# Kernel optimization log

Measured on AMD Instinct MI355X. Metric: run time of the kernel, lower is better.

Reference implementation:

```python
import jax, jax.numpy as jnp
import numpy as np

D = 128      # internal_dimensions
L = 4        # num_edge_convs
N = 100000   # nodes
E = 800000   # edges
G = 64       # graphs
IN = 4       # in_channels


def _ln(x, g, b):
    m = jnp.mean(x, -1, keepdims=True)
    v = jnp.mean((x - m) ** 2, -1, keepdims=True)
    return (x - m) * jax.lax.rsqrt(v + 1e-5) * g + b


def _gelu(x):
    return jax.nn.gelu(x, approximate=False)  # torch nn.GELU default (erf)


def _seg_mean(x, seg, n):
    s = jax.ops.segment_sum(x, seg, num_segments=n)
    c = jax.ops.segment_sum(jnp.ones((x.shape[0], 1), x.dtype), seg, num_segments=n)
    return s / jnp.maximum(c, 1.0)


def _seg_max(x, seg, n):
    m = jax.ops.segment_max(x, seg, num_segments=n)
    return jnp.where(jnp.isfinite(m), m, 0.0)  # empty segments -> 0 (PyG convention)


def _forward(x, edge_index, batch, num_graphs,
             in_W1, in_b1, in_g1, in_bn1, in_W2, in_b2, in_g2, in_bn2,
             pre_g, pre_b, cW1, cb1, cg1, cbb1, cW2, cb2, cg2, cbb2, pW, pb,
             ag_g, ag_b,
             kW1, kb1, kg1, kbb1, kW2, kb2, kg2, kbb2,
             kW3, kb3, kg3, kbb3, kW4, kb4):
    n = x.shape[0]
    # input_net: Linear -> LN -> GELU -> Linear -> LN   (dropout=0, eval)
    h = _gelu(_ln(x @ in_W1 + in_b1, in_g1, in_bn1))
    h = _ln(h @ in_W2 + in_b2, in_g2, in_bn2)

    x_in_max = _seg_max(h, batch, num_graphs)
    x_in_mean = _seg_mean(h, batch, num_graphs)

    src, dst = edge_index[0], edge_index[1]  # PyG: message from src (x_j) to dst (x_i)
    xcur = h
    for l in range(L):
        identity = xcur
        hn = _ln(xcur, pre_g[l], pre_b[l])
        xi = hn[dst]            # [E, D]
        xj = hn[src]            # [E, D]
        m = jnp.concatenate([xi, xj - xi], axis=-1)       # [E, 2D]
        m = _gelu(_ln(m @ cW1[l] + cb1[l], cg1[l], cbb1[l]))
        m = _gelu(_ln(m @ cW2[l] + cb2[l], cg2[l], cbb2[l]))
        a_max = _seg_max(m, dst, n)
        a_mean = _seg_mean(m, dst, n)
        aggr = jnp.concatenate([a_max, a_mean], axis=-1)  # [N, 2D]
        xcur = identity + aggr @ pW[l] + pb[l]

    xcur = _ln(xcur, ag_g, ag_b)
    x_g_max = _seg_max(xcur, batch, num_graphs)
    x_g_mean = _seg_mean(xcur, batch, num_graphs)

    xp = jnp.concatenate([x_in_max, x_in_mean, x_g_max, x_g_mean], axis=-1)  # [G, 4D]
    z = _gelu(_ln(xp @ kW1 + kb1, kg1, kbb1))
    z = _gelu(_ln(z @ kW2 + kb2, kg2, kbb2))
    z = _gelu(_ln(z @ kW3 + kb3, kg3, kbb3))
    return z @ kW4 + kb4  # [G, 1]


def setup_inputs() -> dict:
    key = jax.random.key(0)
    ks = iter(jax.random.split(key, 64))
    def W(shape, fan):
        return jax.random.normal(next(ks), shape, jnp.float32) * np.float32((2.0 / fan) ** 0.5)
    inp = {}
    inp["x"] = jax.random.normal(next(ks), (N, IN), jnp.float32)
    inp["edge_index"] = jax.random.randint(next(ks), (2, E), 0, N)
    inp["batch"] = jnp.sort(jax.random.randint(next(ks), (N,), 0, G))
    inp["num_graphs"] = G
    inp["in_W1"] = W((IN, D), IN); inp["in_b1"] = jnp.zeros((D,), jnp.float32)
    inp["in_g1"] = jnp.ones((D,), jnp.float32); inp["in_bn1"] = jnp.zeros((D,), jnp.float32)
    inp["in_W2"] = W((D, D), D); inp["in_b2"] = jnp.zeros((D,), jnp.float32)
    inp["in_g2"] = jnp.ones((D,), jnp.float32); inp["in_bn2"] = jnp.zeros((D,), jnp.float32)
    inp["pre_g"] = jnp.ones((L, D), jnp.float32); inp["pre_b"] = jnp.zeros((L, D), jnp.float32)
    inp["cW1"] = W((L, 2 * D, D), 2 * D); inp["cb1"] = jnp.zeros((L, D), jnp.float32)
    inp["cg1"] = jnp.ones((L, D), jnp.float32); inp["cbb1"] = jnp.zeros((L, D), jnp.float32)
    inp["cW2"] = W((L, D, D), D); inp["cb2"] = jnp.zeros((L, D), jnp.float32)
    inp["cg2"] = jnp.ones((L, D), jnp.float32); inp["cbb2"] = jnp.zeros((L, D), jnp.float32)
    inp["pW"] = W((L, 2 * D, D), 2 * D); inp["pb"] = jnp.zeros((L, D), jnp.float32)
    inp["ag_g"] = jnp.ones((D,), jnp.float32); inp["ag_b"] = jnp.zeros((D,), jnp.float32)
    inp["kW1"] = W((4 * D, D), 4 * D); inp["kb1"] = jnp.zeros((D,), jnp.float32)
    inp["kg1"] = jnp.ones((D,), jnp.float32); inp["kbb1"] = jnp.zeros((D,), jnp.float32)
    inp["kW2"] = W((D, D), D); inp["kb2"] = jnp.zeros((D,), jnp.float32)
    inp["kg2"] = jnp.ones((D,), jnp.float32); inp["kbb2"] = jnp.zeros((D,), jnp.float32)
    inp["kW3"] = W((D, D // 4), D); inp["kb3"] = jnp.zeros((D // 4,), jnp.float32)
    inp["kg3"] = jnp.ones((D // 4,), jnp.float32); inp["kbb3"] = jnp.zeros((D // 4,), jnp.float32)
    inp["kW4"] = W((D // 4, 1), D // 4); inp["kb4"] = jnp.zeros((1,), jnp.float32)
    return inp


def reference(x, edge_index, batch, num_graphs,
              in_W1, in_b1, in_g1, in_bn1, in_W2, in_b2, in_g2, in_bn2,
              pre_g, pre_b, cW1, cb1, cg1, cbb1, cW2, cb2, cg2, cbb2, pW, pb,
              ag_g, ag_b,
              kW1, kb1, kg1, kbb1, kW2, kb2, kg2, kbb2,
              kW3, kb3, kg3, kbb3, kW4, kb4):
    return _forward(x, edge_index, batch, num_graphs,
                    in_W1, in_b1, in_g1, in_bn1, in_W2, in_b2, in_g2, in_bn2,
                    pre_g, pre_b, cW1, cb1, cg1, cbb1, cW2, cb2, cg2, cbb2, pW, pb,
                    ag_g, ag_b,
                    kW1, kb1, kg1, kbb1, kW2, kb2, kg2, kbb2,
                    kW3, kb3, kg3, kbb3, kW4, kb4)
```

## Files before the change

### kernel.cpp

```cpp
#include <hip/hip_runtime.h>
#include <hip/hip_bf16.h>
#include <math.h>

__device__ __forceinline__ float geluf(float x) {
    return 0.5f * x * (1.0f + erff(x * 0.70710678118654752f));
}
#define MAPNEGINF 0x007FFFFFu
__device__ __forceinline__ float funmap(unsigned m) {
    return __uint_as_float((m & 0x80000000u) ? (m ^ 0x80000000u) : ~m);
}
__device__ __forceinline__ unsigned fmap(float f) {
    unsigned u = __float_as_uint(f);
    return ((int)u < 0) ? ~u : (u | 0x80000000u);
}
__device__ __forceinline__ float wred64(float v) {
#pragma unroll
    for (int m = 1; m < 64; m <<= 1) v += __shfl_xor(v, m);
    return v;
}
__device__ __forceinline__ unsigned short bf16r(float f) {
    unsigned u = __float_as_uint(f);
    u += 0x7fffu + ((u >> 16) & 1u);
    return (unsigned short)(u >> 16);
}

__device__ __forceinline__ void stage_wq(float* Ws, const float* __restrict__ src, int t) {
#pragma unroll
    for (int it = 0; it < 4; ++it) {
        const int idx = it * 1024 + (t << 2);
        *(float4*)(Ws + idx) = *(const float4*)(src + idx);
    }
}

__device__ __forceinline__ void stage_w2(float* Ws, const float* __restrict__ base,
                                         const float* __restrict__ sub, int t) {
#pragma unroll
    for (int it = 0; it < 4; ++it) {
        const int idx = it * 1024 + (t << 2);
        float4 v = *(const float4*)(base + idx);
        if (sub) {
            const float4 s = *(const float4*)(sub + idx);
            v = make_float4(v.x - s.x, v.y - s.y, v.z - s.z, v.w - s.w);
        }
        *(float4*)(Ws + idx) = v;
    }
}

__device__ __forceinline__ void kloop_q(const float* As, const float* Ws, float (&acc)[4][8],
                                        const int r0, const int ogc, const int kb) {
#pragma unroll
    for (int kk = 0; kk < 32; kk += 4) {
        const float4 a0 = *(const float4*)(As + (r0 + 0) * 132 + kb + kk);
        const float4 a1 = *(const float4*)(As + (r0 + 1) * 132 + kb + kk);
        const float4 a2 = *(const float4*)(As + (r0 + 2) * 132 + kb + kk);
        const float4 a3 = *(const float4*)(As + (r0 + 3) * 132 + kb + kk);
#define MAD8(R, AV)                                                                     \
    {                                                                                   \
        acc[R][0] += (AV)*wA.x; acc[R][1] += (AV)*wA.y; acc[R][2] += (AV)*wA.z;         \
        acc[R][3] += (AV)*wA.w; acc[R][4] += (AV)*wB.x; acc[R][5] += (AV)*wB.y;         \
        acc[R][6] += (AV)*wB.z; acc[R][7] += (AV)*wB.w;                                 \
    }
#define KSTEP(J, C)                                                                     \
    {                                                                                   \
        const float4 wA = *(const float4*)(Ws + (kk + (J)) * 128 + ogc);                \
        const float4 wB = *(const float4*)(Ws + (kk + (J)) * 128 + 64 + ogc);           \
        MAD8(0, a0.C) MAD8(1, a1.C) MAD8(2, a2.C) MAD8(3, a3.C)                         \
    }
        KSTEP(0, x) KSTEP(1, y) KSTEP(2, z) KSTEP(3, w)
#undef KSTEP
#undef MAD8
    }
}

__device__ __forceinline__ void kloop2(const float* As, const float* Ws, float (&acc)[2][8],
                                       const int r0, const int ogc, const int kb) {
#pragma unroll
    for (int kk = 0; kk < 32; kk += 4) {
        const float4 a0 = *(const float4*)(As + (r0 + 0) * 132 + kb + kk);
        const float4 a1 = *(const float4*)(As + (r0 + 1) * 132 + kb + kk);
#define MAD8(R, AV)                                                                     \
    {                                                                                   \
        acc[R][0] += (AV)*wA.x; acc[R][1] += (AV)*wA.y; acc[R][2] += (AV)*wA.z;         \
        acc[R][3] += (AV)*wA.w; acc[R][4] += (AV)*wB.x; acc[R][5] += (AV)*wB.y;         \
        acc[R][6] += (AV)*wB.z; acc[R][7] += (AV)*wB.w;                                 \
    }
#define KSTEP(J, C)                                                                     \
    {                                                                                   \
        const float4 wA = *(const float4*)(Ws + (kk + (J)) * 128 + ogc);                \
        const float4 wB = *(const float4*)(Ws + (kk + (J)) * 128 + 64 + ogc);           \
        MAD8(0, a0.C) MAD8(1, a1.C)                                                     \
    }
        KSTEP(0, x) KSTEP(1, y) KSTEP(2, z) KSTEP(3, w)
#undef KSTEP
#undef MAD8
    }
}

__global__ void k_zero(unsigned* __restrict__ p, int n) {
    const int i = blockIdx.x * 256 + threadIdx.x;
    if (i < n) p[i] = 0u;
}

__global__ void k_copyu(const unsigned* __restrict__ a, const unsigned* __restrict__ b,
                        unsigned* __restrict__ ac, unsigned* __restrict__ bc, int n) {
    const int i = blockIdx.x * 256 + threadIdx.x;
    if (i < n) {
        ac[i] = a[i];
        bc[i] = b[i];
    }
}

__global__ void k_count(const int* __restrict__ ei, unsigned* __restrict__ deg, int E) {
    const int e = blockIdx.x * 256 + threadIdx.x;
// ... 95 lines not shown
                                                const float* __restrict__ bias,
                                                const float* __restrict__ g,
                                                const float* __restrict__ b,
                                                float* __restrict__ C, int n) {
    __shared__ float As[32 * 132];
    __shared__ float Ws[4096];
    const int t = threadIdx.x;
    const int n0 = blockIdx.x * 32;
    {
        const int r = t >> 3, c0 = (t & 7) << 4;
        const int row = n0 + r;
        const bool ok = row < n;
#pragma unroll
        for (int j = 0; j < 4; ++j) {
            const int col = c0 + (j << 2);
            float4 v = make_float4(0.f, 0.f, 0.f, 0.f);
            if (ok) v = *(const float4*)(A + (size_t)row * 128 + col);
            *(float4*)(As + r * 132 + col) = v;
        }
    }
    float acc[2][8];
#pragma unroll
    for (int r = 0; r < 2; ++r)
#pragma unroll
        for (int o = 0; o < 8; ++o) acc[r][o] = 0.f;
    const int og = t & 15, eg = t >> 4;
    const int ogc = og << 2, r0 = eg << 1;
#pragma unroll
    for (int q4 = 0; q4 < 4; ++q4) {
        stage_wq(Ws, W + q4 * 4096, t);
        __syncthreads();
        kloop2(As, Ws, acc, r0, ogc, q4 * 32);
        __syncthreads();
    }
    const float4 bA = *(const float4*)(bias + ogc);
    const float4 bB = *(const float4*)(bias + 64 + ogc);
    const float4 gA = *(const float4*)(g + ogc);
    const float4 gB = *(const float4*)(g + 64 + ogc);
    const float4 lA = *(const float4*)(b + ogc);
    const float4 lB = *(const float4*)(b + 64 + ogc);
#pragma unroll
    for (int r = 0; r < 2; ++r) {
        float v[8];
        v[0] = acc[r][0] + bA.x; v[1] = acc[r][1] + bA.y;
        v[2] = acc[r][2] + bA.z; v[3] = acc[r][3] + bA.w;
        v[4] = acc[r][4] + bB.x; v[5] = acc[r][5] + bB.y;
        v[6] = acc[r][6] + bB.z; v[7] = acc[r][7] + bB.w;
        float s = 0.f, q = 0.f;
#pragma unroll
        for (int o = 0; o < 8; ++o) { s += v[o]; q += v[o] * v[o]; }
#pragma unroll
        for (int m = 1; m < 16; m <<= 1) { s += __shfl_xor(s, m); q += __shfl_xor(q, m); }
        const float mean = s * 0.0078125f;
        const float var = q * 0.0078125f - mean * mean;
        const float rs = rsqrtf(var + 1e-5f);
        const int row = n0 + r0 + r;
        if (row < n) {
            *(float4*)(C + (size_t)row * 128 + ogc) = make_float4(
                (v[0] - mean) * rs * gA.x + lA.x, (v[1] - mean) * rs * gA.y + lA.y,
                (v[2] - mean) * rs * gA.z + lA.z, (v[3] - mean) * rs * gA.w + lA.w);
            *(float4*)(C + (size_t)row * 128 + 64 + ogc) = make_float4(
                (v[4] - mean) * rs * gB.x + lB.x, (v[5] - mean) * rs * gB.y + lB.y,
                (v[6] - mean) * rs * gB.z + lB.z, (v[7] - mean) * rs * gB.w + lB.w);
        }
    }
}

__global__ void k_ln(const float* __restrict__ in, const float* __restrict__ g,
                     const float* __restrict__ b, float* __restrict__ out, int n) {
    const int t = threadIdx.x, lane = t & 63, wave = t >> 6;
    const int d0 = lane << 1;
    const float ga = g[d0], gb = g[d0 + 1], ba = b[d0], bb = b[d0 + 1];
    const int stride = gridDim.x * 4;
    for (int node = blockIdx.x * 4 + wave; node < n; node += stride) {
        const float2 v = *(const float2*)(in + (size_t)node * 128 + d0);
        const float s = wred64(v.x + v.y), q = wred64(v.x * v.x + v.y * v.y);
        const float mean = s * 0.0078125f, var = q * 0.0078125f - mean * mean;
        const float rs = rsqrtf(var + 1e-5f);
        *(float2*)(out + (size_t)node * 128 + d0) =
            make_float2((v.x - mean) * rs * ga + ba, (v.y - mean) * rs * gb + bb);
    }
}

__global__ __launch_bounds__(256, 4) void k_gemmh(const float* __restrict__ A,
                                                  const float* __restrict__ g,
                                                  const float* __restrict__ b,
                                                  const float* __restrict__ wbase,
                                                  const float* __restrict__ wsub,
                                                  const float* __restrict__ bias,
                                                  unsigned short* __restrict__ C, int n) {
    __shared__ float As[32 * 132];
    __shared__ float Ws[4096];
    __shared__ float sg[128], sb[128];
    const int t = threadIdx.x;
    const int n0 = blockIdx.x * 32;
    if (t < 128) { sg[t] = g[t]; sb[t] = b[t]; }
    __syncthreads();
    {
        const int r = t >> 3, c0 = (t & 7) << 4;
        const int row = n0 + r;
        const bool ok = row < n;
        float4 v4[4];
        float s = 0.f, q = 0.f;
        if (ok) {
#pragma unroll
            for (int j = 0; j < 4; ++j) {
                v4[j] = *(const float4*)(A + (size_t)row * 128 + c0 + (j << 2));
                s += v4[j].x + v4[j].y + v4[j].z + v4[j].w;
                q += v4[j].x * v4[j].x + v4[j].y * v4[j].y + v4[j].z * v4[j].z +
                     v4[j].w * v4[j].w;
            }
        } else {
#pragma unroll
            for (int j = 0; j < 4; ++j) v4[j] = make_float4(0.f, 0.f, 0.f, 0.f);
        }
        s += __shfl_xor(s, 1); s += __shfl_xor(s, 2); s += __shfl_xor(s, 4);
        q += __shfl_xor(q, 1); q += __shfl_xor(q, 2); q += __shfl_xor(q, 4);
        const float mean = s * 0.0078125f;
        const float var = q * 0.0078125f - mean * mean;
        const float rs = rsqrtf(var + 1e-5f);
#pragma unroll
        for (int j = 0; j < 4; ++j) {
            const int c = c0 + (j << 2);
            As[r * 132 + c + 0] = (v4[j].x - mean) * rs * sg[c + 0] + sb[c + 0];
            As[r * 132 + c + 1] = (v4[j].y - mean) * rs * sg[c + 1] + sb[c + 1];
            As[r * 132 + c + 2] = (v4[j].z - mean) * rs * sg[c + 2] + sb[c + 2];
            As[r * 132 + c + 3] = (v4[j].w - mean) * rs * sg[c + 3] + sb[c + 3];
        }
    }
    float acc[2][8];
#pragma unroll
    for (int r = 0; r < 2; ++r)
#pragma unroll
        for (int o = 0; o < 8; ++o) acc[r][o] = 0.f;
    const int og = t & 15, eg = t >> 4;
    const int ogc = og << 2, r0 = eg << 1;
#pragma unroll
    for (int q4 = 0; q4 < 4; ++q4) {
        stage_w2(Ws, wbase + q4 * 4096, wsub ? (wsub + q4 * 4096) : (const float*)nullptr, t);
        __syncthreads();
        kloop2(As, Ws, acc, r0, ogc, q4 * 32);
        __syncthreads();
    }
    float4 bA = make_float4(0.f, 0.f, 0.f, 0.f), bB = bA;
    if (bias) {
        bA = *(const float4*)(bias + ogc);
        bB = *(const float4*)(bias + 64 + ogc);
    }
#pragma unroll
    for (int r = 0; r < 2; ++r) {
        const int row = n0 + r0 + r;
        if (row < n) {
            ushort4 u0, u1;
            u0.x = bf16r(acc[r][0] + bA.x); u0.y = bf16r(acc[r][1] + bA.y);
            u0.z = bf16r(acc[r][2] + bA.z); u0.w = bf16r(acc[r][3] + bA.w);
            u1.x = bf16r(acc[r][4] + bB.x); u1.y = bf16r(acc[r][5] + bB.y);
            u1.z = bf16r(acc[r][6] + bB.z); u1.w = bf16r(acc[r][7] + bB.w);
            *(ushort4*)(C + (size_t)row * 128 + ogc) = u0;
            *(ushort4*)(C + (size_t)row * 128 + 64 + ogc) = u1;
        }
    }
}

__global__ __launch_bounds__(256, 2) void k_edge(
    const unsigned short* __restrict__ P, const unsigned short* __restrict__ Q,
    const int* __restrict__ esrc, const int* __restrict__ edst, const float* __restrict__ W2,
    const float* __restrict__ g1, const float* __restrict__ b1, const float* __restrict__ cb2,
    const float* __restrict__ g2, const float* __restrict__ b2,
    const unsigned* __restrict__ rowend, const unsigned* __restrict__ degc,
    float* __restrict__ amax, float* __restrict__ asum, float* __restrict__ recmax,
    float* __restrict__ recsum, int* __restrict__ recid, int E) {
    __shared__ float Us[64 * 132];
    __shared__ float Ws[4096];
    __shared__ int sdst[64], ssrc[64], sdg[64];
    __shared__ float scb2[128], sg2[128], sb2[128];
    const int t = threadIdx.x;
    const int base = blockIdx.x * 512;
    if (t >= 128) {
        const int d = t - 128;
        scb2[d] = cb2[d];
        sg2[d] = g2[d];
        sb2[d] = b2[d];
    }
    const int lane = t & 63, wave = t >> 6;
    const int d0 = lane << 1;
    const float g1a = g1[d0], g1b = g1[d0 + 1], b1a = b1[d0], b1b = b1[d0 + 1];
    const int og = t & 15, eg = t >> 4;
    const int ogc = og << 2, r0 = eg << 2;
    int cur = -1, istart = 0;
    float vmax = -INFINITY, vsum = 0.f;
    int id0 = -1, id1 = -1;

    for (int s8 = 0; s8 < 8; ++s8) {
        const int sb = base + s8 * 64;
        __syncthreads();
        if (t < 64) {
            const int idx = sb + t;
            const int ci = idx < E ? idx : (E - 1);
            ssrc[t] = esrc[ci];
            const int d = edst[ci];
            sdg[t] = d;
            sdst[t] = (idx < E) ? d : -1;
        }
        __syncthreads();
#pragma unroll 4
        for (int p = 0; p < 16; ++p) {
            const int i = (p << 2) + wave;
            const unsigned pu = *(const unsigned*)(P + ((size_t)sdg[i] << 7) + d0);
            const unsigned qu = *(const unsigned*)(Q + ((size_t)ssrc[i] << 7) + d0);
            const float x0 = __uint_as_float(pu << 16) + __uint_as_float(qu << 16);
            const float x1 =
                __uint_as_float(pu & 0xffff0000u) + __uint_as_float(qu & 0xffff0000u);
            const float s = wred64(x0 + x1);
            const float q = wred64(x0 * x0 + x1 * x1);
            const float mean = s * 0.0078125f;
            const float var = q * 0.0078125f - mean * mean;
            const float rs = rsqrtf(var + 1e-5f);
            const float y0 = geluf((x0 - mean) * rs * g1a + b1a);
            const float y1 = geluf((x1 - mean) * rs * g1b + b1b);
            *(float2*)(Us + i * 132 + d0) = make_float2(y0, y1);
        }
        float acc[4][8];
#pragma unroll
        for (int r = 0; r < 4; ++r)
#pragma unroll
            for (int o = 0; o < 8; ++o) acc[r][o] = 0.f;
#pragma unroll
        for (int q4 = 0; q4 < 4; ++q4) {
            stage_wq(Ws, W2 + q4 * 4096, t);
            __syncthreads();
            kloop_q(Us, Ws, acc, r0, ogc, q4 * 32);
            __syncthreads();
        }
#pragma unroll
        for (int r = 0; r < 4; ++r) {
            float v[8];
            float s = 0.f, q = 0.f;
#pragma unroll
            for (int o = 0; o < 8; ++o) {
                const int col = (o < 4) ? (ogc + o) : (64 + ogc + o - 4);
                v[o] = acc[r][o] + scb2[col];
                s += v[o];
                q += v[o] * v[o];
            }
#pragma unroll
            for (int m = 1; m < 16; m <<= 1) { s += __shfl_xor(s, m); q += __shfl_xor(q, m); }
            const float mean = s * 0.0078125f;
            const float var = q * 0.0078125f - mean * mean;
            const float rs = rsqrtf(var + 1e-5f);
#pragma unroll
            for (int o = 0; o < 8; ++o) {
                const int col = (o < 4) ? (ogc + o) : (64 + ogc + o - 4);
                v[o] = geluf((v[o] - mean) * rs * sg2[col] + sb2[col]);
            }
            *(float4*)(Us + (r0 + r) * 132 + ogc) = make_float4(v[0], v[1], v[2], v[3]);
            *(float4*)(Us + (r0 + r) * 132 + 64 + ogc) = make_float4(v[4], v[5], v[6], v[7]);
        }
        __syncthreads();
        if (t < 128) {
            for (int i = 0; i < 64; ++i) {
                const int dn = sdst[i];
                const int gi = s8 * 64 + i;
                if (dn != cur) {
                    if (cur >= 0) {
                        const unsigned re = rowend[cur];
                        const unsigned rs0 = re - degc[cur];
                        const unsigned ps = (unsigned)(base + istart);
                        const unsigned pe = (unsigned)(base + gi);
                        if (ps == rs0 && pe == re) {
                            amax[(size_t)cur * 128 + t] = vmax;
                            asum[(size_t)cur * 128 + t] = vsum;
                        } else {
                            const int slot = (istart == 0) ? 0 : 1;
                            const size_t ro = (size_t)(2 * blockIdx.x + slot) * 128 + t;
                            recmax[ro] = vmax;
                            recsum[ro] = vsum;
                            if (slot == 0) id0 = cur; else id1 = cur;
                        }
                    }
                    cur = dn;
                    istart = gi;
                    vmax = -INFINITY;
                    vsum = 0.f;
                }
                if (dn >= 0) {
                    const float v = Us[i * 132 + t];
                    vmax = fmaxf(vmax, v);
                    vsum += v;
                }
            }
        }
    }
    if (t < 128 && cur >= 0) {
        const int iend = min(512, E - base);
        const unsigned re = rowend[cur];
        const unsigned rs0 = re - degc[cur];
        const unsigned ps = (unsigned)(base + istart);
        const unsigned pe = (unsigned)(base + iend);
        if (ps == rs0 && pe == re) {
            amax[(size_t)cur * 128 + t] = vmax;
            asum[(size_t)cur * 128 + t] = vsum;
        } else {
            const int slot = (istart == 0) ? 0 : 1;
            const size_t ro = (size_t)(2 * blockIdx.x + slot) * 128 + t;
            recmax[ro] = vmax;
            recsum[ro] = vsum;
            if (slot == 0) id0 = cur; else id1 = cur;
        }
    }
    if (t == 0) {
        recid[2 * blockIdx.x] = id0;
        recid[2 * blockIdx.x + 1] = id1;
    }
}

__global__ void k_merge(const unsigned* __restrict__ rowend, const unsigned* __restrict__ degc,
                        const float* __restrict__ recmax, const float* __restrict__ recsum,
                        const int* __restrict__ recid, float* __restrict__ amax,
                        float* __restrict__ asum, int n) {
    const int node = blockIdx.x * 2 + (threadIdx.x >> 7);
    const int t = threadIdx.x & 127;
    if (node >= n) return;
    const unsigned dg = degc[node];
    if (dg == 0u) {
        amax[(size_t)node * 128 + t] = 0.f;
        asum[(size_t)node * 128 + t] = 0.f;
        return;
    }
    const unsigned re = rowend[node], rs = re - dg;
    const int b0 = rs >> 9, b1 = (re - 1) >> 9;
    if (b0 == b1) return;
    float m = -INFINITY, s = 0.f;
    for (int b = b0; b <= b1; ++b) {
#pragma unroll
        for (int sl = 0; sl < 2; ++sl) {
            if (recid[2 * b + sl] == node) {
                const size_t ro = (size_t)(2 * b + sl) * 128 + t;
                m = fmaxf(m, recmax[ro]);
                s += recsum[ro];
            }
        }
    }
    amax[(size_t)node * 128 + t] = m;
    asum[(size_t)node * 128 + t] = s;
}

__global__ __launch_bounds__(256, 4) void k_update(const float* __restrict__ amax,
                                                   const float* __restrict__ asum,
                                                   const unsigned* __restrict__ degc,
                                                   const float* __restrict__ pW,
                                                   const float* __restrict__ pb,
                                                   float* __restrict__ xcur, int n) {
    __shared__ float As[32 * 132];
    __shared__ float Ws[4096];
    const int t = threadIdx.x;
    const int n0 = blockIdx.x * 32;
    const int og = t & 15, eg = t >> 4;
    const int ogc = og << 2, r0 = eg << 1;
    float acc[2][8];
#pragma unroll
    for (int r = 0; r < 2; ++r)
#pragma unroll
        for (int o = 0; o < 8; ++o) acc[r][o] = 0.f;
    const int r = t >> 3, c0 = (t & 7) << 4;
    const int row = n0 + r;
    const bool ok = row < n;
#pragma unroll
    for (int pass = 0; pass < 2; ++pass) {
        if (pass == 0) {
#pragma unroll
            for (int j = 0; j < 4; ++j) {
                const int col = c0 + (j << 2);
                float4 v = make_float4(0.f, 0.f, 0.f, 0.f);
                if (ok) v = *(const float4*)(amax + (size_t)row * 128 + col);
                *(float4*)(As + r * 132 + col) = v;
            }
        } else {
            float inv = 0.f;
            if (ok) {
                const unsigned dv = degc[row];
                inv = 1.f / (float)(dv < 1u ? 1u : dv);
            }
#pragma unroll
            for (int j = 0; j < 4; ++j) {
                const int col = c0 + (j << 2);
                float4 v = make_float4(0.f, 0.f, 0.f, 0.f);
                if (ok) {
                    const float4 sv = *(const float4*)(asum + (size_t)row * 128 + col);
                    v = make_float4(sv.x * inv, sv.y * inv, sv.z * inv, sv.w * inv);
                }
                *(float4*)(As + r * 132 + col) = v;
            }
        }
#pragma unroll
        for (int q4 = 0; q4 < 4; ++q4) {
            stage_wq(Ws, pW + (size_t)(pass * 128 + q4 * 32) * 128, t);
            __syncthreads();
            kloop2(As, Ws, acc, r0, ogc, q4 * 32);
            __syncthreads();
        }
    }
    const float4 bA = *(const float4*)(pb + ogc);
    const float4 bB = *(const float4*)(pb + 64 + ogc);
#pragma unroll
    for (int rr = 0; rr < 2; ++rr) {
        const int orow = n0 + r0 + rr;
        if (orow < n) {
            const float4 x0 = *(const float4*)(xcur + (size_t)orow * 128 + ogc);
            const float4 x1 = *(const float4*)(xcur + (size_t)orow * 128 + 64 + ogc);
            *(float4*)(xcur + (size_t)orow * 128 + ogc) =
                make_float4(x0.x + acc[rr][0] + bA.x, x0.y + acc[rr][1] + bA.y,
                            x0.z + acc[rr][2] + bA.z, x0.w + acc[rr][3] + bA.w);
            *(float4*)(xcur + (size_t)orow * 128 + 64 + ogc) =
                make_float4(x1.x + acc[rr][4] + bB.x, x1.y + acc[rr][5] + bB.y,
                            x1.z + acc[rr][6] + bB.z, x1.w + acc[rr][7] + bB.w);
        }
    }
}

__global__ void k_pool_init(unsigned* __restrict__ gmax1, float* __restrict__ gsum1,
                            unsigned* __restrict__ gcount1, unsigned* __restrict__ gmax2,
                            float* __restrict__ gsum2, unsigned* __restrict__ gcount2, int ng) {
    const int i = blockIdx.x * 256 + threadIdx.x;
    if (i < ng * 128) {
        gmax1[i] = MAPNEGINF;
        gsum1[i] = 0.f;
        gmax2[i] = MAPNEGINF;
        gsum2[i] = 0.f;
    }
    if (i < ng) {
        gcount1[i] = 0u;
        gcount2[i] = 0u;
    }
}

__global__ void k_pool(const float* __restrict__ in, const int* __restrict__ batch,
                       unsigned* __restrict__ gmax, float* __restrict__ gsum,
                       unsigned* __restrict__ gcount, int n) {
    const int t = threadIdx.x;
    if (t >= 128) return;
    const int per = (n + gridDim.x - 1) / gridDim.x;
    const int i0 = blockIdx.x * per;
    const int i1 = min(n, i0 + per);
    if (i0 >= i1) return;
    int cur = batch[i0];
    float vmax = -INFINITY, vsum = 0.f;
    unsigned cnt = 0;
    for (int i = i0; i < i1; ++i) {
        const int g = batch[i];
        if (g != cur) {
            atomicMax(gmax + (size_t)cur * 128 + t, fmap(vmax));
            atomicAdd(gsum + (size_t)cur * 128 + t, vsum);
            if (t == 0) atomicAdd(gcount + cur, cnt);
            cur = g;
            vmax = -INFINITY;
            vsum = 0.f;
            cnt = 0;
        }
        const float v = in[(size_t)i * 128 + t];
        vmax = fmaxf(vmax, v);
        vsum += v;
        cnt++;
    }
    atomicMax(gmax + (size_t)cur * 128 + t, fmap(vmax));
    atomicAdd(gsum + (size_t)cur * 128 + t, vsum);
    if (t == 0) atomicAdd(gcount + cur, cnt);
}

__global__ void k_xp(const unsigned* __restrict__ gmax1, const float* __restrict__ gsum1,
                     const unsigned* __restrict__ gcount1, const unsigned* __restrict__ gmax2,
                     const float* __restrict__ gsum2, const unsigned* __restrict__ gcount2,
                     float* __restrict__ xp) {
    const int g = blockIdx.x, d = threadIdx.x;
    const unsigned c1u = gcount1[g], c2u = gcount2[g];
    const float c1 = (float)(c1u < 1u ? 1u : c1u);
    const float c2 = (float)(c2u < 1u ? 1u : c2u);
    const unsigned m1 = gmax1[g * 128 + d], m2 = gmax2[g * 128 + d];
    xp[g * 512 + d] = (m1 == MAPNEGINF) ? 0.f : funmap(m1);
    xp[g * 512 + 128 + d] = gsum1[g * 128 + d] / c1;
    xp[g * 512 + 256 + d] = (m2 == MAPNEGINF) ? 0.f : funmap(m2);
    xp[g * 512 + 384 + d] = gsum2[g * 128 + d] / c2;
}

__global__ __launch_bounds__(64) void k_know(
    const float* __restrict__ xp, const float* __restrict__ kW1, const float* __restrict__ kb1,
    const float* __restrict__ kg1, const float* __restrict__ kbb1, const float* __restrict__ kW2,
    const float* __restrict__ kb2, const float* __restrict__ kg2, const float* __restrict__ kbb2,
    const float* __restrict__ kW3, const float* __restrict__ kb3, const float* __restrict__ kg3,
    const float* __restrict__ kbb3, const float* __restrict__ kW4, const float* __restrict__ kb4,
    float* __restrict__ out) {
    __shared__ float sh[512];
    __shared__ float s3[32];
    const int l = threadIdx.x, g = blockIdx.x;
    const int d0 = l << 1;
    *(float4*)(sh + l * 8) = *(const float4*)(xp + g * 512 + l * 8);
    *(float4*)(sh + l * 8 + 4) = *(const float4*)(xp + g * 512 + l * 8 + 4);
    __syncthreads();
    float a0 = kb1[d0], a1 = kb1[d0 + 1];
    for (int k = 0; k < 512; ++k) {
        const float u = sh[k];
// ... 68 lines not shown
    const int E = in_sizes[1] / 2;
    const int G = 64;
    const int L = 4;

    const float* x = (const float*)d_in[0];
    const int* ei = (const int*)d_in[1];
    const int* batch = (const int*)d_in[2];
    const float* inW1 = (const float*)d_in[4];
    const float* inb1 = (const float*)d_in[5];
    const float* ing1 = (const float*)d_in[6];
    const float* inbn1 = (const float*)d_in[7];
    const float* inW2 = (const float*)d_in[8];
    const float* inb2 = (const float*)d_in[9];
    const float* ing2 = (const float*)d_in[10];
    const float* inbn2 = (const float*)d_in[11];
    const float* pre_g = (const float*)d_in[12];
    const float* pre_b = (const float*)d_in[13];
    const float* cW1 = (const float*)d_in[14];
    const float* cb1 = (const float*)d_in[15];
    const float* cg1 = (const float*)d_in[16];
    const float* cbb1 = (const float*)d_in[17];
    const float* cW2 = (const float*)d_in[18];
    const float* cb2 = (const float*)d_in[19];
    const float* cg2 = (const float*)d_in[20];
    const float* cbb2 = (const float*)d_in[21];
    const float* pW = (const float*)d_in[22];
    const float* pb = (const float*)d_in[23];
    const float* ag_g = (const float*)d_in[24];
    const float* ag_b = (const float*)d_in[25];
    const float* kW1 = (const float*)d_in[26];
    const float* kb1 = (const float*)d_in[27];
    const float* kg1 = (const float*)d_in[28];
    const float* kbb1 = (const float*)d_in[29];
    const float* kW2 = (const float*)d_in[30];
    const float* kb2 = (const float*)d_in[31];
    const float* kg2 = (const float*)d_in[32];
    const float* kbb2 = (const float*)d_in[33];
    const float* kW3 = (const float*)d_in[34];
    const float* kb3 = (const float*)d_in[35];
    const float* kg3 = (const float*)d_in[36];
    const float* kbb3 = (const float*)d_in[37];
    const float* kW4 = (const float*)d_in[38];
    const float* kb4 = (const float*)d_in[39];
    float* out = (float*)d_out;

    const int nblkE = (E + 511) / 512;

    char* wsb = (char*)d_ws;
    size_t off = 0;
    auto ALC = [&](size_t bytes) {
        void* p = wsb + off;
        off = (off + bytes + 255) & ~(size_t)255;
        return p;
    };
    const size_t NB = (size_t)N * 128 * 4;
    float* xcur = (float*)ALC(NB);
    float* amax = (float*)ALC(NB);
    float* asum = (float*)ALC(NB);
    unsigned short* Pb = (unsigned short*)ALC((size_t)N * 128 * 2);
    unsigned short* Qb = (unsigned short*)ALC((size_t)N * 128 * 2);
    unsigned* deg = (unsigned*)ALC((size_t)N * 4);
    unsigned* cursor = (unsigned*)ALC((size_t)N * 4);
    unsigned* degc = (unsigned*)ALC((size_t)N * 4);
    unsigned* rowend = (unsigned*)ALC((size_t)N * 4);
    unsigned* bsum = (unsigned*)ALC(4096);
    int* esrc = (int*)ALC((size_t)E * 4);
    int* edst = (int*)ALC((size_t)E * 4);
    float* recmax = (float*)ALC((size_t)nblkE * 2 * 128 * 4);
    float* recsum = (float*)ALC((size_t)nblkE * 2 * 128 * 4);
    int* recid = (int*)ALC((size_t)nblkE * 2 * 4);
    unsigned* gmax1 = (unsigned*)ALC((size_t)G * 128 * 4);
    float* gsum1 = (float*)ALC((size_t)G * 128 * 4);
    unsigned* gcount1 = (unsigned*)ALC((size_t)G * 4);
    unsigned* gmax2 = (unsigned*)ALC((size_t)G * 128 * 4);
    float* gsum2 = (float*)ALC((size_t)G * 128 * 4);
    unsigned* gcount2 = (unsigned*)ALC((size_t)G * 4);
    float* xp = (float*)ALC((size_t)G * 512 * 4);

    if (off > ws_size) {
        k_zero<<<(out_size + 255) / 256, 256, 0, stream>>>((unsigned*)d_out, out_size);
        return;
    }

    k_zero<<<(N + 255) / 256, 256, 0, stream>>>(deg, N);
    k_count<<<(E + 255) / 256, 256, 0, stream>>>(ei, deg, E);
    const int nb = (N + 1023) / 1024;
    k_scan1<<<nb, 256, 0, stream>>>(deg, cursor, bsum, N);
    k_scan2<<<1, 256, 0, stream>>>(bsum, nb);
    k_scan3<<<nb, 256, 0, stream>>>(cursor, bsum, N);
    k_scatter<<<(E + 255) / 256, 256, 0, stream>>>(ei, cursor, esrc, edst, E);
    k_copyu<<<(N + 255) / 256, 256, 0, stream>>>(deg, cursor, degc, rowend, N);

    const int grid32 = (N + 31) / 32;
    k_in1<<<1024, 256, 0, stream>>>(x, inW1, inb1, ing1, inbn1, amax, N);
    k_in2<<<grid32, 256, 0, stream>>>(amax, inW2, inb2, ing2, inbn2, xcur, N);
    k_pool_init<<<(G * 128 + 255) / 256, 256, 0, stream>>>(gmax1, gsum1, gcount1, gmax2, gsum2,
                                                           gcount2, G);
    k_pool<<<512, 256, 0, stream>>>(xcur, batch, gmax1, gsum1, gcount1, N);

    for (int l = 0; l < L; ++l) {
        const float* c = cW1 + (size_t)l * 32768;
        k_gemmh<<<grid32, 256, 0, stream>>>(xcur, pre_g + l * 128, pre_b + l * 128, c,
                                            c + 16384, cb1 + l * 128, Pb, N);
        k_gemmh<<<grid32, 256, 0, stream>>>(xcur, pre_g + l * 128, pre_b + l * 128, c + 16384,
                                            (const float*)nullptr, (const float*)nullptr, Qb, N);
        k_edge<<<nblkE, 256, 0, stream>>>(Pb, Qb, esrc, edst, cW2 + (size_t)l * 16384,
                                          cg1 + l * 128, cbb1 + l * 128, cb2 + l * 128,
                                          cg2 + l * 128, cbb2 + l * 128, rowend, degc, amax, asum,
                                          recmax, recsum, recid, E);
        k_merge<<<(N + 1) / 2, 256, 0, stream>>>(rowend, degc, recmax, recsum, recid, amax, asum,
                                                 N);
        k_update<<<grid32, 256, 0, stream>>>(amax, asum, degc, pW + (size_t)l * 32768,
                                             pb + l * 128, xcur, N);
    }

    k_ln<<<1024, 256, 0, stream>>>(xcur, ag_g, ag_b, amax, N);
    k_pool<<<512, 256, 0, stream>>>(amax, batch, gmax2, gsum2, gcount2, N);
    k_xp<<<G, 128, 0, stream>>>(gmax1, gsum1, gcount1, gmax2, gsum2, gcount2, xp);
    k_know<<<G, 64, 0, stream>>>(xp, kW1, kb1, kg1, kbb1, kW2, kb2, kg2, kbb2, kW3, kb3, kg3,
                                 kbb3, kW4, kb4, out);
}
```

Before: 100.3 ms.

## Stage full weight matrices in large dynamic LDS for gemm, edge and update kernels

Adds variants of the per-layer gemm, edge-MLP and update kernels that copy the whole 128x128 weight matrix into about 97KB of dynamic shared memory once per block. This removes the per-quarter stage/sync loop, and the edge kernel reuses the staged weights across all 8 sub-tiles of its 512 edges. The gemm and update kernels also move to 64-row tiles with 4 rows per thread. The cost is fewer resident blocks per CU because of the large LDS footprint, with a fallback to the old kernels if the attribute call fails.

```diff
diff --git a/kernel.cpp b/kernel.cpp
--- a/kernel.cpp
+++ b/kernel.cpp
@@ -24,11 +24,27 @@
     return (unsigned short)(u >> 16);
 }
 
+#define DYN_LDS_BYTES 99328
+
 __device__ __forceinline__ void stage_wq(float* Ws, const float* __restrict__ src, int t) {
 #pragma unroll
     for (int it = 0; it < 4; ++it) {
         const int idx = it * 1024 + (t << 2);
         *(float4*)(Ws + idx) = *(const float4*)(src + idx);
+    }
+}
+
+__device__ __forceinline__ void stage_wfull(float* Ws, const float* __restrict__ base,
+                                            const float* __restrict__ sub, int t) {
+#pragma unroll
+    for (int it = 0; it < 16; ++it) {
+        const int idx = it * 1024 + (t << 2);
+        float4 v = *(const float4*)(base + idx);
+        if (sub) {
+            const float4 s = *(const float4*)(sub + idx);
+            v = make_float4(v.x - s.x, v.y - s.y, v.z - s.z, v.w - s.w);
+        }
+        *(float4*)(Ws + idx) = v;
     }
 }
 
@@ -290,29 +306,32 @@
     }
 }
 
-__global__ __launch_bounds__(256, 4) void k_gemmh(const float* __restrict__ A,
-                                                  const float* __restrict__ g,
-                                                  const float* __restrict__ b,
-                                                  const float* __restrict__ wbase,
-                                                  const float* __restrict__ wsub,
-                                                  const float* __restrict__ bias,
-                                                  unsigned short* __restrict__ C, int n) {
-    __shared__ float As[32 * 132];
-    __shared__ float Ws[4096];
+
+__global__ __launch_bounds__(256) void k_gemmh2(const float* __restrict__ A,
+                                                const float* __restrict__ g,
+                                                const float* __restrict__ b,
+                                                const float* __restrict__ wbase,
+                                                const float* __restrict__ wsub,
+                                                const float* __restrict__ bias,
+                                                unsigned short* __restrict__ C, int n) {
+    extern __shared__ float sm[];
+    float* As = sm;
+    float* Ws = sm + 8448;
     __shared__ float sg[128], sb[128];
     const int t = threadIdx.x;
-    const int n0 = blockIdx.x * 32;
+    const int n0 = blockIdx.x * 64;
     if (t < 128) { sg[t] = g[t]; sb[t] = b[t]; }
+    stage_wfull(Ws, wbase, wsub, t);
     __syncthreads();
     {
-        const int r = t >> 3, c0 = (t & 7) << 4;
+        const int r = t >> 2, c0 = (t & 3) << 5;
         const int row = n0 + r;
         const bool ok = row < n;
-        float4 v4[4];
+        float4 v4[8];
         float s = 0.f, q = 0.f;
         if (ok) {
 #pragma unroll
-            for (int j = 0; j < 4; ++j) {
+            for (int j = 0; j < 8; ++j) {
                 v4[j] = *(const float4*)(A + (size_t)row * 128 + c0 + (j << 2));
                 s += v4[j].x + v4[j].y + v4[j].z + v4[j].w;
                 q += v4[j].x * v4[j].x + v4[j].y * v4[j].y + v4[j].z * v4[j].z +
@@ -320,15 +339,15 @@
             }
         } else {
 #pragma unroll
-            for (int j = 0; j < 4; ++j) v4[j] = make_float4(0.f, 0.f, 0.f, 0.f);
-        }
-        s += __shfl_xor(s, 1); s += __shfl_xor(s, 2); s += __shfl_xor(s, 4);
-        q += __shfl_xor(q, 1); q += __shfl_xor(q, 2); q += __shfl_xor(q, 4);
+            for (int j = 0; j < 8; ++j) v4[j] = make_float4(0.f, 0.f, 0.f, 0.f);
+        }
+        s += __shfl_xor(s, 1); s += __shfl_xor(s, 2);
+        q += __shfl_xor(q, 1); q += __shfl_xor(q, 2);
         const float mean = s * 0.0078125f;
         const float var = q * 0.0078125f - mean * mean;
         const float rs = rsqrtf(var + 1e-5f);
 #pragma unroll
-        for (int j = 0; j < 4; ++j) {
+        for (int j = 0; j < 8; ++j) {
             const int c = c0 + (j << 2);
             As[r * 132 + c + 0] = (v4[j].x - mean) * rs * sg[c + 0] + sb[c + 0];
             As[r * 132 + c + 1] = (v4[j].y - mean) * rs * sg[c + 1] + sb[c + 1];
@@ -336,27 +355,23 @@
             As[r * 132 + c + 3] = (v4[j].w - mean) * rs * sg[c + 3] + sb[c + 3];
         }
     }
-    float acc[2][8];
-#pragma unroll
-    for (int r = 0; r < 2; ++r)
+    __syncthreads();
+    float acc[4][8];
+#pragma unroll
+    for (int r = 0; r < 4; ++r)
 #pragma unroll
         for (int o = 0; o < 8; ++o) acc[r][o] = 0.f;
     const int og = t & 15, eg = t >> 4;
-    const int ogc = og << 2, r0 = eg << 1;
-#pragma unroll
-    for (int q4 = 0; q4 < 4; ++q4) {
-        stage_w2(Ws, wbase + q4 * 4096, wsub ? (wsub + q4 * 4096) : (const float*)nullptr, t);
-        __syncthreads();
-        kloop2(As, Ws, acc, r0, ogc, q4 * 32);
-        __syncthreads();
-    }
+    const int ogc = og << 2, r0 = eg << 2;
+#pragma unroll
+    for (int q4 = 0; q4 < 4; ++q4) kloop_q(As, Ws + q4 * 4096, acc, r0, ogc, q4 * 32);
     float4 bA = make_float4(0.f, 0.f, 0.f, 0.f), bB = bA;
     if (bias) {
         bA = *(const float4*)(bias + ogc);
         bB = *(const float4*)(bias + 64 + ogc);
     }
 #pragma unroll
-    for (int r = 0; r < 2; ++r) {
+    for (int r = 0; r < 4; ++r) {
         const int row = n0 + r0 + r;
         if (row < n) {
             ushort4 u0, u1;
@@ -370,7 +385,7 @@
     }
 }
 
-__global__ __launch_bounds__(256, 2) void k_edge(
+__global__ __launch_bounds__(256) void k_edge2(
     const unsigned short* __restrict__ P, const unsigned short* __restrict__ Q,
     const int* __restrict__ esrc, const int* __restrict__ edst, const float* __restrict__ W2,
     const float* __restrict__ g1, const float* __restrict__ b1, const float* __restrict__ cb2,
@@ -378,12 +393,14 @@
     const unsigned* __restrict__ rowend, const unsigned* __restrict__ degc,
     float* __restrict__ amax, float* __restrict__ asum, float* __restrict__ recmax,
     float* __restrict__ recsum, int* __restrict__ recid, int E) {
-    __shared__ float Us[64 * 132];
-    __shared__ float Ws[4096];
+    extern __shared__ float sm[];
+    float* Us = sm;
+    float* Ws = sm + 8448;
     __shared__ int sdst[64], ssrc[64], sdg[64];
     __shared__ float scb2[128], sg2[128], sb2[128];
     const int t = threadIdx.x;
     const int base = blockIdx.x * 512;
+    stage_wfull(Ws, W2, (const float*)nullptr, t);
     if (t >= 128) {
         const int d = t - 128;
         scb2[d] = cb2[d];
@@ -428,18 +445,15 @@
             const float y1 = geluf((x1 - mean) * rs * g1b + b1b);
             *(float2*)(Us + i * 132 + d0) = make_float2(y0, y1);
         }
+        __syncthreads();
         float acc[4][8];
 #pragma unroll
         for (int r = 0; r < 4; ++r)
 #pragma unroll
             for (int o = 0; o < 8; ++o) acc[r][o] = 0.f;
 #pragma unroll
-        for (int q4 = 0; q4 < 4; ++q4) {
-            stage_wq(Ws, W2 + q4 * 4096, t);
-            __syncthreads();
-            kloop_q(Us, Ws, acc, r0, ogc, q4 * 32);
-            __syncthreads();
-        }
+        for (int q4 = 0; q4 < 4; ++q4) kloop_q(Us, Ws + q4 * 4096, acc, r0, ogc, q4 * 32);
+        __syncthreads();
 #pragma unroll
         for (int r = 0; r < 4; ++r) {
             float v[8];
@@ -522,35 +536,309 @@
     }
 }
 
-__global__ void k_merge(const unsigned* __restrict__ rowend, const unsigned* __restrict__ degc,
-                        const float* __restrict__ recmax, const float* __restrict__ recsum,
-                        const int* __restrict__ recid, float* __restrict__ amax,
-                        float* __restrict__ asum, int n) {
-    const int node = blockIdx.x * 2 + (threadIdx.x >> 7);
-    const int t = threadIdx.x & 127;
-    if (node >= n) return;
-    const unsigned dg = degc[node];
-    if (dg == 0u) {
-        amax[(size_t)node * 128 + t] = 0.f;
-        asum[(size_t)node * 128 + t] = 0.f;
-        return;
-    }
-    const unsigned re = rowend[node], rs = re - dg;
-    const int b0 = rs >> 9, b1 = (re - 1) >> 9;
-    if (b0 == b1) return;
-    float m = -INFINITY, s = 0.f;
-    for (int b = b0; b <= b1; ++b) {
-#pragma unroll
-        for (int sl = 0; sl < 2; ++sl) {
-            if (recid[2 * b + sl] == node) {
-                const size_t ro = (size_t)(2 * b + sl) * 128 + t;
-                m = fmaxf(m, recmax[ro]);
-                s += recsum[ro];
-            }
-        }
-    }
-    amax[(size_t)node * 128 + t] = m;
-    asum[(size_t)node * 128 + t] = s;
+__global__ __launch_bounds__(256) void k_update2(const float* __restrict__ amax,
+                                                 const float* __restrict__ asum,
+                                                 const unsigned* __restrict__ degc,
+                                                 const float* __restrict__ pW,
+                                                 const float* __restrict__ pb,
+                                                 float* __restrict__ xcur, int n) {
+    extern __shared__ float sm[];
+    float* As = sm;
+    float* Ws = sm + 8448;
+    const int t = threadIdx.x;
+    const int n0 = blockIdx.x * 64;
+    const int og = t & 15, eg = t >> 4;
+    const int ogc = og << 2, r0 = eg << 2;
+    float acc[4][8];
+#pragma unroll
+    for (int r = 0; r < 4; ++r)
+#pragma unroll
+        for (int o = 0; o < 8; ++o) acc[r][o] = 0.f;
+    const int r = t >> 2, c0 = (t & 3) << 5;
+    const int row = n0 + r;
+    const bool ok = row < n;
+#pragma unroll
+    for (int pass = 0; pass < 2; ++pass) {
+        if (pass == 1) __syncthreads();
+        if (pass == 0) {
+#pragma unroll
+            for (int j = 0; j < 8; ++j) {
+                const int col = c0 + (j << 2);
+                float4 v = make_float4(0.f, 0.f, 0.f, 0.f);
+                if (ok) v = *(const float4*)(amax + (size_t)row * 128 + col);
+                *(float4*)(As + r * 132 + col) = v;
+            }
+        } else {
+            float inv = 0.f;
+            if (ok) {
+                const unsigned dv = degc[row];
+                inv = 1.f / (float)(dv < 1u ? 1u : dv);
+            }
+#pragma unroll
+            for (int j = 0; j < 8; ++j) {
+                const int col = c0 + (j << 2);
+                float4 v = make_float4(0.f, 0.f, 0.f, 0.f);
+                if (ok) {
+                    const float4 sv = *(const float4*)(asum + (size_t)row * 128 + col);
+                    v = make_float4(sv.x * inv, sv.y * inv, sv.z * inv, sv.w * inv);
+                }
+                *(float4*)(As + r * 132 + col) = v;
+            }
+        }
+        stage_wfull(Ws, pW + (size_t)pass * 16384, (const float*)nullptr, t);
+        __syncthreads();
+#pragma unroll
+        for (int q4 = 0; q4 < 4; ++q4) kloop_q(As, Ws + q4 * 4096, acc, r0, ogc, q4 * 32);
+    }
+    const float4 bA = *(const float4*)(pb + ogc);
+    const float4 bB = *(const float4*)(pb + 64 + ogc);
+#pragma unroll
+    for (int rr = 0; rr < 4; ++rr) {
+        const int orow = n0 + r0 + rr;
+        if (orow < n) {
+            const float4 x0 = *(const float4*)(xcur + (size_t)orow * 128 + ogc);
+            const float4 x1 = *(const float4*)(xcur + (size_t)orow * 128 + 64 + ogc);
+            *(float4*)(xcur + (size_t)orow * 128 + ogc) =
+                make_float4(x0.x + acc[rr][0] + bA.x, x0.y + acc[rr][1] + bA.y,
+                            x0.z + acc[rr][2] + bA.z, x0.w + acc[rr][3] + bA.w);
+            *(float4*)(xcur + (size_t)orow * 128 + 64 + ogc) =
+                make_float4(x1.x + acc[rr][4] + bB.x, x1.y + acc[rr][5] + bB.y,
+                            x1.z + acc[rr][6] + bB.z, x1.w + acc[rr][7] + bB.w);
+        }
+    }
+}
+
+
+__global__ __launch_bounds__(256, 4) void k_gemmh(const float* __restrict__ A,
+                                                  const float* __restrict__ g,
+                                                  const float* __restrict__ b,
+                                                  const float* __restrict__ wbase,
+                                                  const float* __restrict__ wsub,
+                                                  const float* __restrict__ bias,
+                                                  unsigned short* __restrict__ C, int n) {
+    __shared__ float As[32 * 132];
+    __shared__ float Ws[4096];
+    __shared__ float sg[128], sb[128];
+    const int t = threadIdx.x;
+    const int n0 = blockIdx.x * 32;
+    if (t < 128) { sg[t] = g[t]; sb[t] = b[t]; }
+    __syncthreads();
+    {
+        const int r = t >> 3, c0 = (t & 7) << 4;
+        const int row = n0 + r;
+        const bool ok = row < n;
+        float4 v4[4];
+        float s = 0.f, q = 0.f;
+        if (ok) {
+#pragma unroll
+            for (int j = 0; j < 4; ++j) {
+                v4[j] = *(const float4*)(A + (size_t)row * 128 + c0 + (j << 2));
+                s += v4[j].x + v4[j].y + v4[j].z + v4[j].w;
+                q += v4[j].x * v4[j].x + v4[j].y * v4[j].y + v4[j].z * v4[j].z +
+                     v4[j].w * v4[j].w;
+            }
+        } else {
+#pragma unroll
+            for (int j = 0; j < 4; ++j) v4[j] = make_float4(0.f, 0.f, 0.f, 0.f);
+        }
+        s += __shfl_xor(s, 1); s += __shfl_xor(s, 2); s += __shfl_xor(s, 4);
+        q += __shfl_xor(q, 1); q += __shfl_xor(q, 2); q += __shfl_xor(q, 4);
+        const float mean = s * 0.0078125f;
+        const float var = q * 0.0078125f - mean * mean;
+        const float rs = rsqrtf(var + 1e-5f);
+#pragma unroll
+        for (int j = 0; j < 4; ++j) {
+            const int c = c0 + (j << 2);
+            As[r * 132 + c + 0] = (v4[j].x - mean) * rs * sg[c + 0] + sb[c + 0];
+            As[r * 132 + c + 1] = (v4[j].y - mean) * rs * sg[c + 1] + sb[c + 1];
+            As[r * 132 + c + 2] = (v4[j].z - mean) * rs * sg[c + 2] + sb[c + 2];
+            As[r * 132 + c + 3] = (v4[j].w - mean) * rs * sg[c + 3] + sb[c + 3];
+        }
+    }
+    float acc[2][8];
+#pragma unroll
+    for (int r = 0; r < 2; ++r)
+#pragma unroll
+        for (int o = 0; o < 8; ++o) acc[r][o] = 0.f;
+    const int og = t & 15, eg = t >> 4;
+    const int ogc = og << 2, r0 = eg << 1;
+#pragma unroll
+    for (int q4 = 0; q4 < 4; ++q4) {
+        stage_w2(Ws, wbase + q4 * 4096, wsub ? (wsub + q4 * 4096) : (const float*)nullptr, t);
+        __syncthreads();
+        kloop2(As, Ws, acc, r0, ogc, q4 * 32);
+        __syncthreads();
+    }
+    float4 bA = make_float4(0.f, 0.f, 0.f, 0.f), bB = bA;
+    if (bias) {
+        bA = *(const float4*)(bias + ogc);
+        bB = *(const float4*)(bias + 64 + ogc);
+    }
+#pragma unroll
+    for (int r = 0; r < 2; ++r) {
+        const int row = n0 + r0 + r;
+        if (row < n) {
+            ushort4 u0, u1;
+            u0.x = bf16r(acc[r][0] + bA.x); u0.y = bf16r(acc[r][1] + bA.y);
+            u0.z = bf16r(acc[r][2] + bA.z); u0.w = bf16r(acc[r][3] + bA.w);
+            u1.x = bf16r(acc[r][4] + bB.x); u1.y = bf16r(acc[r][5] + bB.y);
+            u1.z = bf16r(acc[r][6] + bB.z); u1.w = bf16r(acc[r][7] + bB.w);
+            *(ushort4*)(C + (size_t)row * 128 + ogc) = u0;
+            *(ushort4*)(C + (size_t)row * 128 + 64 + ogc) = u1;
+        }
+    }
+}
+
+__global__ __launch_bounds__(256, 2) void k_edge(
+    const unsigned short* __restrict__ P, const unsigned short* __restrict__ Q,
+    const int* __restrict__ esrc, const int* __restrict__ edst, const float* __restrict__ W2,
+    const float* __restrict__ g1, const float* __restrict__ b1, const float* __restrict__ cb2,
+    const float* __restrict__ g2, const float* __restrict__ b2,
+    const unsigned* __restrict__ rowend, const unsigned* __restrict__ degc,
+    float* __restrict__ amax, float* __restrict__ asum, float* __restrict__ recmax,
+    float* __restrict__ recsum, int* __restrict__ recid, int E) {
+    __shared__ float Us[64 * 132];
+    __shared__ float Ws[4096];
+    __shared__ int sdst[64], ssrc[64], sdg[64];
+    __shared__ float scb2[128], sg2[128], sb2[128];
+    const int t = threadIdx.x;
+    const int base = blockIdx.x * 512;
+    if (t >= 128) {
+        const int d = t - 128;
+        scb2[d] = cb2[d];
+        sg2[d] = g2[d];
+        sb2[d] = b2[d];
+    }
+    const int lane = t & 63, wave = t >> 6;
+    const int d0 = lane << 1;
+    const float g1a = g1[d0], g1b = g1[d0 + 1], b1a = b1[d0], b1b = b1[d0 + 1];
+    const int og = t & 15, eg = t >> 4;
+    const int ogc = og << 2, r0 = eg << 2;
+    int cur = -1, istart = 0;
+    float vmax = -INFINITY, vsum = 0.f;
+    int id0 = -1, id1 = -1;
+
+    for (int s8 = 0; s8 < 8; ++s8) {
+        const int sb = base + s8 * 64;
+        __syncthreads();
+        if (t < 64) {
+            const int idx = sb + t;
+            const int ci = idx < E ? idx : (E - 1);
+            ssrc[t] = esrc[ci];
+            const int d = edst[ci];
+            sdg[t] = d;
+            sdst[t] = (idx < E) ? d : -1;
+        }
+        __syncthreads();
+#pragma unroll 4
+        for (int p = 0; p < 16; ++p) {
+            const int i = (p << 2) + wave;
+            const unsigned pu = *(const unsigned*)(P + ((size_t)sdg[i] << 7) + d0);
+            const unsigned qu = *(const unsigned*)(Q + ((size_t)ssrc[i] << 7) + d0);
+            const float x0 = __uint_as_float(pu << 16) + __uint_as_float(qu << 16);
+            const float x1 =
+                __uint_as_float(pu & 0xffff0000u) + __uint_as_float(qu & 0xffff0000u);
+            const float s = wred64(x0 + x1);
+            const float q = wred64(x0 * x0 + x1 * x1);
+            const float mean = s * 0.0078125f;
+            const float var = q * 0.0078125f - mean * mean;
+            const float rs = rsqrtf(var + 1e-5f);
+            const float y0 = geluf((x0 - mean) * rs * g1a + b1a);
+            const float y1 = geluf((x1 - mean) * rs * g1b + b1b);
+            *(float2*)(Us + i * 132 + d0) = make_float2(y0, y1);
+        }
+        float acc[4][8];
+#pragma unroll
+        for (int r = 0; r < 4; ++r)
+#pragma unroll
+            for (int o = 0; o < 8; ++o) acc[r][o] = 0.f;
+#pragma unroll
+        for (int q4 = 0; q4 < 4; ++q4) {
+            stage_wq(Ws, W2 + q4 * 4096, t);
+            __syncthreads();
+            kloop_q(Us, Ws, acc, r0, ogc, q4 * 32);
+            __syncthreads();
+        }
+#pragma unroll
+        for (int r = 0; r < 4; ++r) {
+            float v[8];
+            float s = 0.f, q = 0.f;
+#pragma unroll
+            for (int o = 0; o < 8; ++o) {
+                const int col = (o < 4) ? (ogc + o) : (64 + ogc + o - 4);
+                v[o] = acc[r][o] + scb2[col];
+                s += v[o];
+                q += v[o] * v[o];
+            }
+#pragma unroll
+            for (int m = 1; m < 16; m <<= 1) { s += __shfl_xor(s, m); q += __shfl_xor(q, m); }
+            const float mean = s * 0.0078125f;
+            const float var = q * 0.0078125f - mean * mean;
+            const float rs = rsqrtf(var + 1e-5f);
+#pragma unroll
+            for (int o = 0; o < 8; ++o) {
+                const int col = (o < 4) ? (ogc + o) : (64 + ogc + o - 4);
+                v[o] = geluf((v[o] - mean) * rs * sg2[col] + sb2[col]);
+            }
+            *(float4*)(Us + (r0 + r) * 132 + ogc) = make_float4(v[0], v[1], v[2], v[3]);
+            *(float4*)(Us + (r0 + r) * 132 + 64 + ogc) = make_float4(v[4], v[5], v[6], v[7]);
+        }
+        __syncthreads();
+        if (t < 128) {
+            for (int i = 0; i < 64; ++i) {
+                const int dn = sdst[i];
+                const int gi = s8 * 64 + i;
+                if (dn != cur) {
+                    if (cur >= 0) {
+                        const unsigned re = rowend[cur];
+                        const unsigned rs0 = re - degc[cur];
+                        const unsigned ps = (unsigned)(base + istart);
+                        const unsigned pe = (unsigned)(base + gi);
+                        if (ps == rs0 && pe == re) {
+                            amax[(size_t)cur * 128 + t] = vmax;
+                            asum[(size_t)cur * 128 + t] = vsum;
+                        } else {
+                            const int slot = (istart == 0) ? 0 : 1;
+                            const size_t ro = (size_t)(2 * blockIdx.x + slot) * 128 + t;
+                            recmax[ro] = vmax;
+                            recsum[ro] = vsum;
+                            if (slot == 0) id0 = cur; else id1 = cur;
+                        }
+                    }
+                    cur = dn;
+                    istart = gi;
+                    vmax = -INFINITY;
+                    vsum = 0.f;
+                }
+                if (dn >= 0) {
+                    const float v = Us[i * 132 + t];
+                    vmax = fmaxf(vmax, v);
+                    vsum += v;
+                }
+            }
+        }
+    }
+    if (t < 128 && cur >= 0) {
+        const int iend = min(512, E - base);
+        const unsigned re = rowend[cur];
+        const unsigned rs0 = re - degc[cur];
+        const unsigned ps = (unsigned)(base + istart);
+        const unsigned pe = (unsigned)(base + iend);
+        if (ps == rs0 && pe == re) {
+            amax[(size_t)cur * 128 + t] = vmax;
+            asum[(size_t)cur * 128 + t] = vsum;
+        } else {
+            const int slot = (istart == 0) ? 0 : 1;
+            const size_t ro = (size_t)(2 * blockIdx.x + slot) * 128 + t;
+            recmax[ro] = vmax;
+            recsum[ro] = vsum;
+            if (slot == 0) id0 = cur; else id1 = cur;
+        }
+    }
+    if (t == 0) {
+        recid[2 * blockIdx.x] = id0;
+        recid[2 * blockIdx.x + 1] = id1;
+    }
 }
 
 __global__ __launch_bounds__(256, 4) void k_update(const float* __restrict__ amax,
@@ -624,6 +912,37 @@
                             x1.z + acc[rr][6] + bB.z, x1.w + acc[rr][7] + bB.w);
         }
     }
+}
+
+__global__ void k_merge(const unsigned* __restrict__ rowend, const unsigned* __restrict__ degc,
+                        const float* __restrict__ recmax, const float* __restrict__ recsum,
+                        const int* __restrict__ recid, float* __restrict__ amax,
+                        float* __restrict__ asum, int n) {
+    const int node = blockIdx.x * 2 + (threadIdx.x >> 7);
+    const int t = threadIdx.x & 127;
+    if (node >= n) return;
+    const unsigned dg = degc[node];
+    if (dg == 0u) {
+        amax[(size_t)node * 128 + t] = 0.f;
+        asum[(size_t)node * 128 + t] = 0.f;
+        return;
+    }
+    const unsigned re = rowend[node], rs = re - dg;
+    const int b0 = rs >> 9, b1 = (re - 1) >> 9;
+    if (b0 == b1) return;
+    float m = -INFINITY, s = 0.f;
+    for (int b = b0; b <= b1; ++b) {
+#pragma unroll
+        for (int sl = 0; sl < 2; ++sl) {
+            if (recid[2 * b + sl] == node) {
+                const size_t ro = (size_t)(2 * b + sl) * 128 + t;
+                m = fmaxf(m, recmax[ro]);
+                s += recsum[ro];
+            }
+        }
+    }
+    amax[(size_t)node * 128 + t] = m;
+    asum[(size_t)node * 128 + t] = s;
 }
 
 __global__ void k_pool_init(unsigned* __restrict__ gmax1, float* __restrict__ gsum1,
@@ -858,6 +1177,14 @@
         return;
     }
 
+    const hipError_t eA = hipFuncSetAttribute(
+        (const void*)k_edge2, hipFuncAttributeMaxDynamicSharedMemorySize, DYN_LDS_BYTES);
+    const hipError_t eB = hipFuncSetAttribute(
+        (const void*)k_gemmh2, hipFuncAttributeMaxDynamicSharedMemorySize, DYN_LDS_BYTES);
+    const hipError_t eC = hipFuncSetAttribute(
+        (const void*)k_update2, hipFuncAttributeMaxDynamicSharedMemorySize, DYN_LDS_BYTES);
+    const bool big = (eA == hipSuccess && eB == hipSuccess && eC == hipSuccess);
+
     k_zero<<<(N + 255) / 256, 256, 0, stream>>>(deg, N);
     k_count<<<(E + 255) / 256, 256, 0, stream>>>(ei, deg, E);
     const int nb = (N + 1023) / 1024;
@@ -868,6 +1195,7 @@
     k_copyu<<<(N + 255) / 256, 256, 0, stream>>>(deg, cursor, degc, rowend, N);
 
     const int grid32 = (N + 31) / 32;
+    const int grid64 = (N + 63) / 64;
     k_in1<<<1024, 256, 0, stream>>>(x, inW1, inb1, ing1, inbn1, amax, N);
     k_in2<<<grid32, 256, 0, stream>>>(amax, inW2, inb2, ing2, inbn2, xcur, N);
     k_pool_init<<<(G * 128 + 255) / 256, 256, 0, stream>>>(gmax1, gsum1, gcount1, gmax2, gsum2,
@@ -876,18 +1204,35 @@
 
     for (int l = 0; l < L; ++l) {
         const float* c = cW1 + (size_t)l * 32768;
-        k_gemmh<<<grid32, 256, 0, stream>>>(xcur, pre_g + l * 128, pre_b + l * 128, c,
-                                            c + 16384, cb1 + l * 128, Pb, N);
-        k_gemmh<<<grid32, 256, 0, stream>>>(xcur, pre_g + l * 128, pre_b + l * 128, c + 16384,
-                                            (const float*)nullptr, (const float*)nullptr, Qb, N);
-        k_edge<<<nblkE, 256, 0, stream>>>(Pb, Qb, esrc, edst, cW2 + (size_t)l * 16384,
-                                          cg1 + l * 128, cbb1 + l * 128, cb2 + l * 128,
-                                          cg2 + l * 128, cbb2 + l * 128, rowend, degc, amax, asum,
-                                          recmax, recsum, recid, E);
-        k_merge<<<(N + 1) / 2, 256, 0, stream>>>(rowend, degc, recmax, recsum, recid, amax, asum,
-                                                 N);
-        k_update<<<grid32, 256, 0, stream>>>(amax, asum, degc, pW + (size_t)l * 32768,
-                                             pb + l * 128, xcur, N);
+        if (big) {
+            k_gemmh2<<<grid64, 256, DYN_LDS_BYTES, stream>>>(
+                xcur, pre_g + l * 128, pre_b + l * 128, c, c + 16384, cb1 + l * 128, Pb, N);
+            k_gemmh2<<<grid64, 256, DYN_LDS_BYTES, stream>>>(
+                xcur, pre_g + l * 128, pre_b + l * 128, c + 16384, (const float*)nullptr,
+                (const float*)nullptr, Qb, N);
+            k_edge2<<<nblkE, 256, DYN_LDS_BYTES, stream>>>(
+                Pb, Qb, esrc, edst, cW2 + (size_t)l * 16384, cg1 + l * 128, cbb1 + l * 128,
+                cb2 + l * 128, cg2 + l * 128, cbb2 + l * 128, rowend, degc, amax, asum, recmax,
+                recsum, recid, E);
+            k_merge<<<(N + 1) / 2, 256, 0, stream>>>(rowend, degc, recmax, recsum, recid, amax,
+                                                     asum, N);
+            k_update2<<<grid64, 256, DYN_LDS_BYTES, stream>>>(
+                amax, asum, degc, pW + (size_t)l * 32768, pb + l * 128, xcur, N);
+        } else {
+            k_gemmh<<<grid32, 256, 0, stream>>>(xcur, pre_g + l * 128, pre_b + l * 128, c,
+                                                c + 16384, cb1 + l * 128, Pb, N);
+            k_gemmh<<<grid32, 256, 0, stream>>>(xcur, pre_g + l * 128, pre_b + l * 128,
+                                                c + 16384, (const float*)nullptr,
+                                                (const float*)nullptr, Qb, N);
+            k_edge<<<nblkE, 256, 0, stream>>>(Pb, Qb, esrc, edst, cW2 + (size_t)l * 16384,
+                                              cg1 + l * 128, cbb1 + l * 128, cb2 + l * 128,
+                                              cg2 + l * 128, cbb2 + l * 128, rowend, degc, amax,
+                                              asum, recmax, recsum, recid, E);
+            k_merge<<<(N + 1) / 2, 256, 0, stream>>>(rowend, degc, recmax, recsum, recid, amax,
+                                                     asum, N);
+            k_update<<<grid32, 256, 0, stream>>>(amax, asum, degc, pW + (size_t)l * 32768,
+                                                 pb + l * 128, xcur, N);
+        }
     }
 
     k_ln<<<1024, 256, 0, stream>>>(xcur, ag_g, ag_b, amax, N);
```

New measurement: 98.63 ms. Within noise of the previous version (-1.7%).
